# Kernel tuning notes

Measured on AMD Instinct MI355X. Metric: run time of the kernel, lower is better.

The kernel has to match this reference:

```python
import jax, jax.numpy as jnp
import numpy as np

N_MOL, P_PRO, HID, HEADS, B = 2048, 2048, 64, 16, 64


def setup_inputs() -> dict:
    key = jax.random.key(0)
    ks = jax.random.split(key, 9)
    s = 0.1  # weight scale
    return {
        "mol_feats": jax.random.normal(ks[0], (N_MOL, HID), jnp.float32),
        "fused_feats": jax.random.normal(ks[1], (P_PRO, HID), jnp.float32),
        "Wmu": jax.random.normal(ks[2], (2 * HID, HEADS), jnp.float32) * s,
        "bmu": jax.random.normal(ks[3], (HEADS,), jnp.float32) * s,
        "W1": jax.random.normal(ks[4], (HEADS, 2 * HEADS), jnp.float32) * s,
        "b1": jax.random.normal(ks[5], (2 * HEADS,), jnp.float32) * s,
        "W2": jax.random.normal(ks[6], (2 * HEADS, 1), jnp.float32) * s,
        "b2": jax.random.normal(ks[7], (1,), jnp.float32) * s,
        "mol_batch": jnp.sort(jax.random.randint(ks[8], (N_MOL,), 0, B)).astype(jnp.int64),
        "num_graphs": B,
    }


def reference(mol_feats, fused_feats, Wmu, bmu, W1, b1, W2, b2, mol_batch, num_graphs):
    H = mol_feats.shape[1]
    # In the torch code: atom_pairs = cat([mol_feats[mol_index], fused_feats[pro_index]])
    # with mol_index/pro_index forming the full ligand-atom x protein-atom cross product.
    # Split the Linear weight so cat+gather becomes a broadcast sum (same math).
    a_mol = mol_feats @ Wmu[:H] + bmu          # [N, heads]
    a_pro = fused_feats @ Wmu[H:]              # [P, heads]
    mu = jax.nn.elu(a_mol[:, None, :] + a_pro[None, :, :]) + 1.0  # [N, P, heads]
    # scatter_sum over mol_index == sum over all protein atoms per ligand atom
    y_atom = jnp.sum(mu, axis=1)               # [N, heads]
    # scatter_sum over mol_batch: atom -> graph
    y = jax.ops.segment_sum(y_atom, mol_batch, num_segments=num_graphs) * 0.001  # [B, heads]
    y = jax.nn.elu(y @ W1 + b1)
    return y @ W2 + b2                          # [B, 1]
```

## Files before the change

kernel.cpp:

```cpp
#include <hip/hip_runtime.h>

#define N_MOL 2048
#define P_PRO 2048
#define HID   64
#define HEADS 16
#define NGRAPH 64

#define OFF_PEPRO 65536
#define OFF_YPART 131072

__global__ __launch_bounds__(256) void k1_proj(
    const float* __restrict__ mol, const float* __restrict__ pro,
    const float* __restrict__ Wmu, const float* __restrict__ bmu,
    float* __restrict__ ws)
{
    __shared__ float fs[16 * 64];
    __shared__ float wsh[64 * 16];
    const int tid = threadIdx.x;
    const int blk = blockIdx.x;
    const bool isMol = blk < (N_MOL / 16);
    const int rowbase = (isMol ? blk : blk - (N_MOL / 16)) * 16;
    const float* feats = isMol ? (mol + rowbase * HID) : (pro + rowbase * HID);
    const float* wsrc  = Wmu + (isMol ? 0 : HID * HEADS);

    ((float4*)fs)[tid]  = ((const float4*)feats)[tid];
    ((float4*)wsh)[tid] = ((const float4*)wsrc)[tid];
    __syncthreads();

    const int h = tid & 15, r = tid >> 4;
    float acc = isMol ? bmu[h] : 0.0f;
#pragma unroll
    for (int k = 0; k < 64; ++k)
        acc += fs[r * 64 + k] * wsh[k * 16 + h];

    float2* pe = (float2*)(ws + (isMol ? 0 : OFF_PEPRO));
    const int idx = (rowbase + r) * 16 + h;
    float2 v; v.x = acc; v.y = __expf(acc);
    pe[idx] = v;
}

__global__ __launch_bounds__(256) void k2_pair(
    const float* __restrict__ ws_in, float* __restrict__ y_part)
{
    const float2* pe_mol = (const float2*)ws_in;
    const float2* pe_pro = (const float2*)(ws_in + OFF_PEPRO);

    const int tid = threadIdx.x;
    const int h = tid & 15, g = tid >> 4;
    const int nt = blockIdx.x >> 2, pt = blockIdx.x & 3;
    const int nbase = nt * 8;
    const int pflat = pt * (512 * 16);

    float a1[8], ea[8], acc[8];
#pragma unroll
    for (int j = 0; j < 8; ++j) {
        const float2 m = pe_mol[(nbase + j) * 16 + h];
        a1[j]  = m.x + 1.0f;
        ea[j]  = m.y;
        acc[j] = 0.0f;
    }

#pragma unroll 4
    for (int i = 0; i < 32; ++i) {
        const float2 p = pe_pro[pflat + i * 256 + tid];
        const float bp = p.x, eb = p.y;
#pragma unroll
        for (int j = 0; j < 8; ++j) {
            const float s1 = a1[j] + bp;
            const float e  = ea[j] * eb;
            acc[j] += (s1 > 1.0f) ? s1 : e;
        }
    }

    __shared__ float red[8 * 16 * 16];
#pragma unroll
    for (int j = 0; j < 8; ++j)
        red[j * 256 + g * 16 + h] = acc[j];
    __syncthreads();
    if (tid < 128) {
        const int j = tid >> 4, hh = tid & 15;
        float s = 0.0f;
#pragma unroll
        for (int g2 = 0; g2 < 16; ++g2)
            s += red[j * 256 + g2 * 16 + hh];
        y_part[pt * 32768 + (nbase + j) * 16 + hh] = s;
    }
}

__global__ __launch_bounds__(256) void k3_seg_mlp(
    const float* __restrict__ y_part, const int* __restrict__ batch,
    const float* __restrict__ W1, const float* __restrict__ b1,
    const float* __restrict__ W2, const float* __restrict__ b2,
    float* __restrict__ out)
{
    const int tid = threadIdx.x;
    const int b = blockIdx.x;
    __shared__ int s_start, s_end;
    if (tid == 0) { s_start = 0; s_end = 0; }
    __syncthreads();

    for (int i = tid; i < N_MOL; i += 256) {
        const int bi = batch[i];
        if (bi == b) {
            if (i == 0 || batch[i - 1] != b) s_start = i;
            if (i == N_MOL - 1 || batch[i + 1] != b) s_end = i + 1;
        }
    }
    __syncthreads();

    const int h = tid & 15, rr = tid >> 4;
    float s = 0.0f;
    for (int n = s_start + rr; n < s_end; n += 16) {
        const int o = n * 16 + h;
        s += y_part[o] + y_part[32768 + o] + y_part[65536 + o] + y_part[98304 + o];
    }

    __shared__ float red[256];
    __shared__ float ysum[HEADS];
    red[tid] = s;
    __syncthreads();
    if (tid < 16) {
        float c = 0.0f;
#pragma unroll
        for (int r2 = 0; r2 < 16; ++r2) c += red[r2 * 16 + tid];
        ysum[tid] = c * 0.001f;
    }
    __syncthreads();

    if (tid < 32) {
        const int j = tid;
        float t = b1[j];
#pragma unroll
        for (int hh = 0; hh < HEADS; ++hh) t += ysum[hh] * W1[hh * 32 + j];
        t = (t > 0.0f) ? t : (__expf(t) - 1.0f);
        float v = t * W2[j];
#pragma unroll
        for (int off = 16; off > 0; off >>= 1) v += __shfl_down(v, off, 32);
        if (tid == 0) out[b] = v + b2[0];
    }
}

extern "C" void kernel_launch(void* const* d_in, const int* in_sizes, int n_in,
                              void* d_out, int out_size, void* d_ws, size_t ws_size,
                              hipStream_t stream) {
    const float* mol   = (const float*)d_in[0];
    const float* pro   = (const float*)d_in[1];
    const float* Wmu   = (const float*)d_in[2];
    const float* bmu   = (const float*)d_in[3];
    const float* W1    = (const float*)d_in[4];
    const float* b1    = (const float*)d_in[5];
    const float* W2    = (const float*)d_in[6];
    const float* b2    = (const float*)d_in[7];
    const int*   batch = (const int*)d_in[8];
    float* ws = (float*)d_ws;

    hipLaunchKernelGGL(k1_proj, dim3(256), dim3(256), 0, stream,
                       mol, pro, Wmu, bmu, ws);
    hipLaunchKernelGGL(k2_pair, dim3(1024), dim3(256), 0, stream,
                       ws, ws + OFF_YPART);
    hipLaunchKernelGGL(k3_seg_mlp, dim3(NGRAPH), dim3(256), 0, stream,
                       ws + OFF_YPART, batch, W1, b1, W2, b2, (float*)d_out);
}
```

Baseline: 86.86 us.

## Fuse segment-sum MLP into pair kernel via last-block atomic, vectorize pair loop

Removes the third kernel launch by having the last-finishing pair block, found through an atomic counter, perform the segment sum and the MLP. Segment boundaries come from a binary search over batch ids staged in shared memory. The pair loop now loads float4 so each thread handles two heads, and the ELU select is replaced with a single fmed3 instruction. The tail stage now runs in one block, which serializes the reduction over 64 graphs, and the fused kernel carries extra shared memory that may lower occupancy.

```diff
diff --git a/kernel.cpp b/kernel.cpp
--- a/kernel.cpp
+++ b/kernel.cpp
@@ -8,6 +8,7 @@
 
 #define OFF_PEPRO 65536
 #define OFF_YPART 131072
+#define OFF_CNT   262144
 
 __global__ __launch_bounds__(256) void k1_proj(
     const float* __restrict__ mol, const float* __restrict__ pro,
@@ -18,6 +19,8 @@
     __shared__ float wsh[64 * 16];
     const int tid = threadIdx.x;
     const int blk = blockIdx.x;
+    if (blk == 0 && tid == 0) ((int*)(ws + OFF_CNT))[0] = 0;
+
     const bool isMol = blk < (N_MOL / 16);
     const int rowbase = (isMol ? blk : blk - (N_MOL / 16)) * 16;
     const float* feats = isMol ? (mol + rowbase * HID) : (pro + rowbase * HID);
@@ -40,103 +43,103 @@
 }
 
 __global__ __launch_bounds__(256) void k2_pair(
-    const float* __restrict__ ws_in, float* __restrict__ y_part)
+    const float* __restrict__ ws_in, const int* __restrict__ batch,
+    const float* __restrict__ W1, const float* __restrict__ b1,
+    const float* __restrict__ W2, const float* __restrict__ b2,
+    float* __restrict__ y_part, int* __restrict__ cnt,
+    float* __restrict__ out)
 {
-    const float2* pe_mol = (const float2*)ws_in;
-    const float2* pe_pro = (const float2*)(ws_in + OFF_PEPRO);
+    const float4* pe_mol4 = (const float4*)ws_in;
+    const float4* pe_pro4 = (const float4*)(ws_in + OFF_PEPRO);
 
     const int tid = threadIdx.x;
-    const int h = tid & 15, g = tid >> 4;
+    const int hf = tid & 7;
     const int nt = blockIdx.x >> 2, pt = blockIdx.x & 3;
     const int nbase = nt * 8;
-    const int pflat = pt * (512 * 16);
+    const int pbase4 = pt * 4096;
 
-    float a1[8], ea[8], acc[8];
+    float a10[8], a11[8], ea0[8], ea1[8], acc0[8], acc1[8];
 #pragma unroll
     for (int j = 0; j < 8; ++j) {
-        const float2 m = pe_mol[(nbase + j) * 16 + h];
-        a1[j]  = m.x + 1.0f;
-        ea[j]  = m.y;
-        acc[j] = 0.0f;
+        const float4 m = pe_mol4[(nbase + j) * 8 + hf];
+        a10[j] = m.x + 1.0f; ea0[j] = m.y;
+        a11[j] = m.z + 1.0f; ea1[j] = m.w;
+        acc0[j] = 0.0f; acc1[j] = 0.0f;
     }
 
 #pragma unroll 4
-    for (int i = 0; i < 32; ++i) {
-        const float2 p = pe_pro[pflat + i * 256 + tid];
-        const float bp = p.x, eb = p.y;
+    for (int i = 0; i < 16; ++i) {
+        const float4 p = pe_pro4[pbase4 + i * 256 + tid];
 #pragma unroll
         for (int j = 0; j < 8; ++j) {
-            const float s1 = a1[j] + bp;
-            const float e  = ea[j] * eb;
-            acc[j] += (s1 > 1.0f) ? s1 : e;
+            acc0[j] += __builtin_amdgcn_fmed3f(a10[j] + p.x, ea0[j] * p.y, 1.0f);
+            acc1[j] += __builtin_amdgcn_fmed3f(a11[j] + p.z, ea1[j] * p.w, 1.0f);
         }
     }
 
-    __shared__ float red[8 * 16 * 16];
+    __shared__ float red[8 * 32 * 16];
 #pragma unroll
     for (int j = 0; j < 8; ++j)
-        red[j * 256 + g * 16 + h] = acc[j];
+        ((float2*)red)[j * 256 + tid] = make_float2(acc0[j], acc1[j]);
     __syncthreads();
     if (tid < 128) {
         const int j = tid >> 4, hh = tid & 15;
         float s = 0.0f;
 #pragma unroll
-        for (int g2 = 0; g2 < 16; ++g2)
-            s += red[j * 256 + g2 * 16 + hh];
+        for (int g2 = 0; g2 < 32; ++g2)
+            s += red[j * 512 + g2 * 16 + hh];
         y_part[pt * 32768 + (nbase + j) * 16 + hh] = s;
     }
-}
 
-__global__ __launch_bounds__(256) void k3_seg_mlp(
-    const float* __restrict__ y_part, const int* __restrict__ batch,
-    const float* __restrict__ W1, const float* __restrict__ b1,
-    const float* __restrict__ W2, const float* __restrict__ b2,
-    float* __restrict__ out)
-{
-    const int tid = threadIdx.x;
-    const int b = blockIdx.x;
-    __shared__ int s_start, s_end;
-    if (tid == 0) { s_start = 0; s_end = 0; }
+    __threadfence();
     __syncthreads();
+    __shared__ int s_last;
+    if (tid == 0) s_last = (atomicAdd(cnt, 1) == (int)gridDim.x - 1) ? 1 : 0;
+    __syncthreads();
+    if (!s_last) return;
+    __threadfence();
 
-    for (int i = tid; i < N_MOL; i += 256) {
-        const int bi = batch[i];
-        if (bi == b) {
-            if (i == 0 || batch[i - 1] != b) s_start = i;
-            if (i == N_MOL - 1 || batch[i + 1] != b) s_end = i + 1;
-        }
+    __shared__ int sb[N_MOL];
+    for (int i = tid; i < N_MOL; i += 256) sb[i] = batch[i];
+    __syncthreads();
+    __shared__ int bnd[NGRAPH + 1];
+    if (tid <= NGRAPH) {
+        const int b = tid;
+        int lo = 0, hi = N_MOL;
+        while (lo < hi) { const int mid = (lo + hi) >> 1;
+                          if (sb[mid] < b) lo = mid + 1; else hi = mid; }
+        bnd[b] = lo;
     }
     __syncthreads();
 
-    const int h = tid & 15, rr = tid >> 4;
-    float s = 0.0f;
-    for (int n = s_start + rr; n < s_end; n += 16) {
-        const int o = n * 16 + h;
-        s += y_part[o] + y_part[32768 + o] + y_part[65536 + o] + y_part[98304 + o];
-    }
-
-    __shared__ float red[256];
-    __shared__ float ysum[HEADS];
-    red[tid] = s;
-    __syncthreads();
-    if (tid < 16) {
-        float c = 0.0f;
+    __shared__ float ysum[NGRAPH * HEADS];
 #pragma unroll
-        for (int r2 = 0; r2 < 16; ++r2) c += red[r2 * 16 + tid];
-        ysum[tid] = c * 0.001f;
+    for (int k = 0; k < 4; ++k) {
+        const int task = tid + k * 256;
+        const int b = task >> 4, hh = task & 15;
+        const int s0 = bnd[b], e0 = bnd[b + 1];
+        float s = 0.0f;
+        for (int n = s0; n < e0; ++n) {
+            const int o = n * 16 + hh;
+            s += (y_part[o] + y_part[32768 + o]) +
+                 (y_part[65536 + o] + y_part[98304 + o]);
+        }
+        ysum[b * 16 + hh] = s * 0.001f;
     }
     __syncthreads();
 
-    if (tid < 32) {
-        const int j = tid;
+    const int j = tid & 31, grp = tid >> 5;
+#pragma unroll
+    for (int bb = 0; bb < 8; ++bb) {
+        const int b = grp * 8 + bb;
         float t = b1[j];
 #pragma unroll
-        for (int hh = 0; hh < HEADS; ++hh) t += ysum[hh] * W1[hh * 32 + j];
+        for (int hh = 0; hh < HEADS; ++hh) t += ysum[b * 16 + hh] * W1[hh * 32 + j];
         t = (t > 0.0f) ? t : (__expf(t) - 1.0f);
         float v = t * W2[j];
 #pragma unroll
         for (int off = 16; off > 0; off >>= 1) v += __shfl_down(v, off, 32);
-        if (tid == 0) out[b] = v + b2[0];
+        if (j == 0) out[b] = v + b2[0];
     }
 }
 
@@ -157,7 +160,6 @@
     hipLaunchKernelGGL(k1_proj, dim3(256), dim3(256), 0, stream,
                        mol, pro, Wmu, bmu, ws);
     hipLaunchKernelGGL(k2_pair, dim3(1024), dim3(256), 0, stream,
-                       ws, ws + OFF_YPART);
-    hipLaunchKernelGGL(k3_seg_mlp, dim3(NGRAPH), dim3(256), 0, stream,
-                       ws + OFF_YPART, batch, W1, b1, W2, b2, (float*)d_out);
+                       ws, batch, W1, b1, W2, b2,
+                       ws + OFF_YPART, (int*)(ws + OFF_CNT), (float*)d_out);
 }
```

After: 197.5 us. 127% more time.
